# Kernel tuning notes

Measured on AMD Instinct MI355X. Metric: run time of the kernel, lower is better.

The kernel has to match this reference:

```python
import jax, jax.numpy as jnp
import numpy as np
from jax.scipy.fft import dct

B, C, H, W = 64, 3, 512, 512


def dct2(x):
    # 2D DCT-II with ortho norm, matching scipy.fft.dct applied on axis=-1 then axis=-2
    x = dct(x, type=2, norm='ortho', axis=-1)
    x = dct(x, type=2, norm='ortho', axis=-2)
    return x


def setup_inputs() -> dict:
    key = jax.random.key(0)
    k1, k2, k3, k4 = jax.random.split(key, 4)
    return {
        'x': jax.random.normal(k1, (B, C, H, W), dtype=jnp.float32),
        'attention': jax.random.uniform(k2, (H, W), dtype=jnp.float32),
        'row_weights': jax.random.uniform(k3, (H,), dtype=jnp.float32),
        'col_weights': jax.random.uniform(k4, (W,), dtype=jnp.float32),
    }


def reference(x, attention, row_weights, col_weights):
    xd = dct2(x)                       # [B, C, H, W]
    gray = xd.mean(axis=1)             # [B, H, W] (channel mean)
    weighted = gray * attention        # [B, H, W]
    row_sum = weighted.mean(axis=2)    # [B, H] mean over W
    col_sum = weighted.mean(axis=1)    # [B, W] mean over H
    row_out = (row_sum * row_weights).mean(axis=1)  # [B]
    col_out = (col_sum * col_weights).mean(axis=1)  # [B]
    return jax.nn.sigmoid(jnp.stack([col_out, row_out], axis=1))  # [B, 2]
```

## Files before the change

kernel.cpp:

```cpp
#include <hip/hip_runtime.h>
#include <math.h>

#define NN 512
#define MM (NN * NN)
#define HW (NN * NN)
#define CH 3

__device__ __forceinline__ float dct_s(int k) {
    return (k == 0) ? 0.04419417382415922f : 0.0625f;
}

__global__ void __launch_bounds__(256) k_stageA(
    const float* __restrict__ att, const float* __restrict__ rw,
    const float* __restrict__ cw, float* __restrict__ Tr, float* __restrict__ Tc)
{
    __shared__ float sD[2048];
    __shared__ float sRw[512];
    __shared__ float sAcc[256 * 9];
    const int tid = threadIdx.x;
    const int bx  = blockIdx.x;
    const int h0  = (bx >> 3) * 4;
    const int wp0 = (bx & 7) * 64;
    const int kc  = tid >> 6;
    const int wl  = tid & 63;
    const int wp  = wp0 + wl;
    const int hp0 = kc * 128;

    #pragma unroll
    for (int e = 0; e < 8; ++e) {
        int idx = tid * 8 + e;
        int hp = idx >> 2, i = idx & 3;
        int m = ((2 * (h0 + i) + 1) * hp) & 2047;
        sD[idx] = dct_s(hp) * cospif((float)m * (1.0f / 1024.0f));
    }
    sRw[tid] = rw[tid];
    sRw[256 + tid] = rw[256 + tid];
    __syncthreads();

    float ar0=0.f,ar1=0.f,ar2=0.f,ar3=0.f, as0=0.f,as1=0.f,as2=0.f,as3=0.f;
    #pragma unroll 4
    for (int t = 0; t < 128; ++t) {
        int hp = hp0 + t;
        float a = att[hp * NN + wp];
        float r = sRw[hp];
        float4 d = *reinterpret_cast<const float4*>(&sD[hp * 4]);
        float ra = r * a;
        ar0 += d.x * ra; as0 += d.x * a;
        ar1 += d.y * ra; as1 += d.y * a;
        ar2 += d.z * ra; as2 += d.z * a;
        ar3 += d.w * ra; as3 += d.w * a;
    }
    float* sa = &sAcc[tid * 9];
    sa[0]=ar0; sa[1]=ar1; sa[2]=ar2; sa[3]=ar3;
    sa[4]=as0; sa[5]=as1; sa[6]=as2; sa[7]=as3;
    __syncthreads();
    if (tid < 64) {
        float v[8];
        #pragma unroll
        for (int j = 0; j < 8; ++j)
            v[j] = sAcc[(0*64 + tid)*9 + j] + sAcc[(1*64 + tid)*9 + j]
                 + sAcc[(2*64 + tid)*9 + j] + sAcc[(3*64 + tid)*9 + j];
        float c = cw[wp0 + tid];
        #pragma unroll
        for (int i = 0; i < 4; ++i) {
            Tr[(h0 + i) * NN + wp0 + tid] = v[i];
            Tc[(h0 + i) * NN + wp0 + tid] = v[4 + i] * c;
        }
    }
}

__global__ void __launch_bounds__(256) k_stageB(
    const float* __restrict__ Tr, const float* __restrict__ Tc,
    float* __restrict__ Gr, float* __restrict__ Gc)
{
    __shared__ float sT[512 * 8];
    __shared__ float sAcc[256 * 9];
    const int tid = threadIdx.x;
    const int bx  = blockIdx.x;
    const int h0  = (bx >> 3) * 4;
    const int w0  = (bx & 7) * 64;
    const int kc  = tid >> 6;
    const int wl  = tid & 63;
    const int w   = w0 + wl;
    const int wp0 = kc * 128;

    #pragma unroll
    for (int i = 0; i < 4; ++i) {
        sT[tid * 8 + i]             = Tr[(h0 + i) * NN + tid];
        sT[tid * 8 + 4 + i]         = Tc[(h0 + i) * NN + tid];
        sT[(tid + 256) * 8 + i]     = Tr[(h0 + i) * NN + tid + 256];
        sT[(tid + 256) * 8 + 4 + i] = Tc[(h0 + i) * NN + tid + 256];
    }
    __syncthreads();

    float gr0=0.f,gr1=0.f,gr2=0.f,gr3=0.f, gc0=0.f,gc1=0.f,gc2=0.f,gc3=0.f;
    const int w2 = 2 * w + 1;
    int m = (w2 * wp0) & 2047;
    #pragma unroll 4
    for (int t = 0; t < 128; ++t) {
        int wp = wp0 + t;
        float s = (wp == 0) ? 0.04419417382415922f : 0.0625f;
        float d = s * cospif((float)m * (1.0f / 1024.0f));
        m = (m + w2) & 2047;
        float4 ta = *reinterpret_cast<const float4*>(&sT[wp * 8]);
        float4 tb = *reinterpret_cast<const float4*>(&sT[wp * 8 + 4]);
        gr0 += ta.x * d; gr1 += ta.y * d; gr2 += ta.z * d; gr3 += ta.w * d;
        gc0 += tb.x * d; gc1 += tb.y * d; gc2 += tb.z * d; gc3 += tb.w * d;
    }
    float* sa = &sAcc[tid * 9];
    sa[0]=gr0; sa[1]=gr1; sa[2]=gr2; sa[3]=gr3;
    sa[4]=gc0; sa[5]=gc1; sa[6]=gc2; sa[7]=gc3;
    __syncthreads();
    if (tid < 64) {
        float v[8];
        #pragma unroll
        for (int j = 0; j < 8; ++j)
            v[j] = sAcc[(0*64 + tid)*9 + j] + sAcc[(1*64 + tid)*9 + j]
                 + sAcc[(2*64 + tid)*9 + j] + sAcc[(3*64 + tid)*9 + j];
        #pragma unroll
        for (int i = 0; i < 4; ++i) {
            Gr[(h0 + i) * NN + w0 + tid] = v[i];
            Gc[(h0 + i) * NN + w0 + tid] = v[4 + i];
        }
    }
}

__global__ void __launch_bounds__(256, 4) k_reduce(
    const float* __restrict__ x, const float* __restrict__ Gr,
    const float* __restrict__ Gc, float* __restrict__ partials)
{
    const int ck = blockIdx.x;
    const int bc = blockIdx.y;
    const int t  = threadIdx.x;
    const float* xp = x + (size_t)bc * HW;
    const int base = ck * (HW / 32) + t * 4;

    float accr = 0.f, accc = 0.f;
    #pragma unroll
    for (int j = 0; j < 8; ++j) {
        int hw = base + j * 1024;
        float4 xv = *(const float4*)(xp + hw);
        float4 gr = *(const float4*)(Gr + hw);
        float4 gc = *(const float4*)(Gc + hw);
        accr += gr.x * xv.x + gr.y * xv.y + gr.z * xv.z + gr.w * xv.w;
        accc += gc.x * xv.x + gc.y * xv.y + gc.z * xv.z + gc.w * xv.w;
    }
    for (int off = 32; off > 0; off >>= 1) {
        accr += __shfl_down(accr, off);
        accc += __shfl_down(accc, off);
    }
    __shared__ float sr[4], sc[4];
    int wid = t >> 6;
    if ((t & 63) == 0) { sr[wid] = accr; sc[wid] = accc; }
    __syncthreads();
    if (t == 0) {
        partials[(bc * 32 + ck) * 2 + 0] = sr[0] + sr[1] + sr[2] + sr[3];
        partials[(bc * 32 + ck) * 2 + 1] = sc[0] + sc[1] + sc[2] + sc[3];
    }
}

__global__ void k_final(const float* __restrict__ partials, float* __restrict__ out) {
    int b = threadIdx.x;
    float r = 0.f, c = 0.f;
    #pragma unroll
    for (int i = 0; i < 96; ++i) {
        r += partials[(b * 96 + i) * 2 + 0];
        c += partials[(b * 96 + i) * 2 + 1];
    }
    const float inv = 1.0f / (float)(CH * HW);
    r *= inv; c *= inv;
    out[b * 2 + 0] = 1.0f / (1.0f + expf(-c));
    out[b * 2 + 1] = 1.0f / (1.0f + expf(-r));
}

extern "C" void kernel_launch(void* const* d_in, const int* in_sizes, int n_in,
                              void* d_out, int out_size, void* d_ws, size_t ws_size,
                              hipStream_t stream) {
    const float* x   = (const float*)d_in[0];
    const float* att = (const float*)d_in[1];
    const float* rw  = (const float*)d_in[2];
    const float* cw  = (const float*)d_in[3];
    float* out = (float*)d_out;

    float* ws = (float*)d_ws;
    float* Tr = ws;
    float* Tc = ws + 1 * MM;
    float* Gr = ws + 2 * MM;
    float* Gc = ws + 3 * MM;
    float* partials = ws + 4 * MM;

    k_stageA<<<1024, 256, 0, stream>>>(att, rw, cw, Tr, Tc);
    k_stageB<<<1024, 256, 0, stream>>>(Tr, Tc, Gr, Gc);
    dim3 g(32, 192);
    k_reduce<<<g, 256, 0, stream>>>(x, Gr, Gc, partials);
    k_final<<<1, 64, 0, stream>>>(partials, out);
}
```

Baseline: 85.59 us.

## Reuse DCT weight slices across batches and channels in the reduction kernel

```diff
diff --git a/kernel.cpp b/kernel.cpp
--- a/kernel.cpp
+++ b/kernel.cpp
@@ -125,37 +125,69 @@
     }
 }
 
-__global__ void __launch_bounds__(256, 4) k_reduce(
+#define DOT(g, v) (g.x*v.x + g.y*v.y + g.z*v.z + g.w*v.w)
+#define PLANE(AR, AC, XP) do {                                   \
+    float4 v0 = *(const float4*)(XP);                            \
+    float4 v1 = *(const float4*)((XP) + 1024);                   \
+    float4 v2 = *(const float4*)((XP) + 2048);                   \
+    float4 v3 = *(const float4*)((XP) + 3072);                   \
+    AR += DOT(gr0, v0) + DOT(gr1, v1) + DOT(gr2, v2) + DOT(gr3, v3); \
+    AC += DOT(gc0, v0) + DOT(gc1, v1) + DOT(gc2, v2) + DOT(gc3, v3); \
+} while (0)
+
+__global__ void __launch_bounds__(256) k_reduce(
     const float* __restrict__ x, const float* __restrict__ Gr,
     const float* __restrict__ Gc, float* __restrict__ partials)
 {
     const int ck = blockIdx.x;
-    const int bc = blockIdx.y;
+    const int bg = blockIdx.y;
     const int t  = threadIdx.x;
-    const float* xp = x + (size_t)bc * HW;
-    const int base = ck * (HW / 32) + t * 4;
-
-    float accr = 0.f, accc = 0.f;
-    #pragma unroll
-    for (int j = 0; j < 8; ++j) {
-        int hw = base + j * 1024;
-        float4 xv = *(const float4*)(xp + hw);
-        float4 gr = *(const float4*)(Gr + hw);
-        float4 gc = *(const float4*)(Gc + hw);
-        accr += gr.x * xv.x + gr.y * xv.y + gr.z * xv.z + gr.w * xv.w;
-        accc += gc.x * xv.x + gc.y * xv.y + gc.z * xv.z + gc.w * xv.w;
-    }
+    const int base = ck * 4096 + t * 4;
+
+    float4 gr0 = *(const float4*)(Gr + base);
+    float4 gr1 = *(const float4*)(Gr + base + 1024);
+    float4 gr2 = *(const float4*)(Gr + base + 2048);
+    float4 gr3 = *(const float4*)(Gr + base + 3072);
+    float4 gc0 = *(const float4*)(Gc + base);
+    float4 gc1 = *(const float4*)(Gc + base + 1024);
+    float4 gc2 = *(const float4*)(Gc + base + 2048);
+    float4 gc3 = *(const float4*)(Gc + base + 3072);
+
+    const size_t b0 = (size_t)bg * 4;
+    float ar0=0.f, ar1=0.f, ar2=0.f, ar3=0.f;
+    float ac0=0.f, ac1=0.f, ac2=0.f, ac3=0.f;
+    #pragma unroll
+    for (int c = 0; c < 3; ++c) {
+        const float* xp0 = x + ((b0 + 0) * 3 + c) * HW + base;
+        const float* xp1 = x + ((b0 + 1) * 3 + c) * HW + base;
+        const float* xp2 = x + ((b0 + 2) * 3 + c) * HW + base;
+        const float* xp3 = x + ((b0 + 3) * 3 + c) * HW + base;
+        PLANE(ar0, ac0, xp0);
+        PLANE(ar1, ac1, xp1);
+        PLANE(ar2, ac2, xp2);
+        PLANE(ar3, ac3, xp3);
+    }
+
+    #pragma unroll
     for (int off = 32; off > 0; off >>= 1) {
-        accr += __shfl_down(accr, off);
-        accc += __shfl_down(accc, off);
-    }
-    __shared__ float sr[4], sc[4];
+        ar0 += __shfl_down(ar0, off);  ac0 += __shfl_down(ac0, off);
+        ar1 += __shfl_down(ar1, off);  ac1 += __shfl_down(ac1, off);
+        ar2 += __shfl_down(ar2, off);  ac2 += __shfl_down(ac2, off);
+        ar3 += __shfl_down(ar3, off);  ac3 += __shfl_down(ac3, off);
+    }
+    __shared__ float sm[4][8];
     int wid = t >> 6;
-    if ((t & 63) == 0) { sr[wid] = accr; sc[wid] = accc; }
-    __syncthreads();
-    if (t == 0) {
-        partials[(bc * 32 + ck) * 2 + 0] = sr[0] + sr[1] + sr[2] + sr[3];
-        partials[(bc * 32 + ck) * 2 + 1] = sc[0] + sc[1] + sc[2] + sc[3];
+    if ((t & 63) == 0) {
+        sm[wid][0] = ar0; sm[wid][1] = ac0; sm[wid][2] = ar1; sm[wid][3] = ac1;
+        sm[wid][4] = ar2; sm[wid][5] = ac2; sm[wid][6] = ar3; sm[wid][7] = ac3;
+    }
+    __syncthreads();
+    if (t < 4) {
+        float r = sm[0][t*2]   + sm[1][t*2]   + sm[2][t*2]   + sm[3][t*2];
+        float c = sm[0][t*2+1] + sm[1][t*2+1] + sm[2][t*2+1] + sm[3][t*2+1];
+        int b = bg * 4 + t;
+        partials[(b * 64 + ck) * 2 + 0] = r;
+        partials[(b * 64 + ck) * 2 + 1] = c;
     }
 }
 
@@ -163,9 +195,9 @@
     int b = threadIdx.x;
     float r = 0.f, c = 0.f;
     #pragma unroll
-    for (int i = 0; i < 96; ++i) {
-        r += partials[(b * 96 + i) * 2 + 0];
-        c += partials[(b * 96 + i) * 2 + 1];
+    for (int i = 0; i < 64; ++i) {
+        r += partials[(b * 64 + i) * 2 + 0];
+        c += partials[(b * 64 + i) * 2 + 1];
     }
     const float inv = 1.0f / (float)(CH * HW);
     r *= inv; c *= inv;
@@ -191,7 +223,7 @@
 
     k_stageA<<<1024, 256, 0, stream>>>(att, rw, cw, Tr, Tc);
     k_stageB<<<1024, 256, 0, stream>>>(Tr, Tc, Gr, Gc);
-    dim3 g(32, 192);
+    dim3 g(64, 16);
     k_reduce<<<g, 256, 0, stream>>>(x, Gr, Gc, partials);
     k_final<<<1, 64, 0, stream>>>(partials, out);
 }
```

Result: slower. 88.35 us (+3.2%).
